# Performance work log

Measured on AMD Instinct MI355X. Metric: run time of the kernel, lower is better.

## Reference

```python
import math
import jax, jax.numpy as jnp
import numpy as np

B = 8          # number of graphs in the batch
NMAX = 256     # max nodes per graph (padding size)
K = 128        # num_kernels
H = 32         # num_heads
NTYPE = 101    # max_node_type + 1


def setup_inputs() -> dict:
    key = jax.random.key(0)
    ks = jax.random.split(key, 10)
    sizes = np.asarray(NMAX - np.arange(B) * 16, dtype=np.int32)  # 256,240,...,144 -> ragged
    N = int(sizes.sum())  # 1600
    coord = jax.random.normal(ks[0], (N, 3), dtype=jnp.float32) * 3.0
    node_type = jax.random.randint(ks[1], (N,), 0, NTYPE, dtype=jnp.int32)
    gaussian_means = jax.random.uniform(ks[2], (1, K), minval=0.0, maxval=3.0, dtype=jnp.float32)
    gaussian_stds = jax.random.uniform(ks[3], (1, K), minval=0.0, maxval=3.0, dtype=jnp.float32)
    # nn.Embedding(max_node_type+1, 2) tables; original init is const(0)/const(1),
    # we perturb so the computation is non-degenerate.
    mul_w = jax.random.normal(ks[4], (NTYPE, 2), dtype=jnp.float32) * 0.1
    bias_w = 1.0 + jax.random.normal(ks[5], (NTYPE, 2), dtype=jnp.float32) * 0.1
    W1 = jax.random.normal(ks[6], (K, K), dtype=jnp.float32) / math.sqrt(K)
    b1 = jnp.zeros((K,), dtype=jnp.float32)
    W2 = jax.random.normal(ks[7], (K, H), dtype=jnp.float32) / math.sqrt(K)
    b2 = jnp.zeros((H,), dtype=jnp.float32)
    return {
        "coord": coord,
        "gaussian_means": gaussian_means,
        "gaussian_stds": gaussian_stds,
        "mul_w": mul_w,
        "bias_w": bias_w,
        "W1": W1,
        "b1": b1,
        "W2": W2,
        "b2": b2,
        "node_type": node_type,
        "batch_num_nodes": jnp.asarray(sizes),
    }


def reference(coord, gaussian_means, gaussian_stds, mul_w, bias_w, W1, b1, W2, b2,
              node_type, batch_num_nodes):
    N = coord.shape[0]
    offsets = jnp.concatenate([jnp.zeros((1,), dtype=batch_num_nodes.dtype),
                               jnp.cumsum(batch_num_nodes)[:-1]])
    ar = jnp.arange(NMAX)
    idx = offsets[:, None] + ar[None, :]                     # [B, n] flat node index per graph slot
    valid = ar[None, :] < batch_num_nodes[:, None]           # [B, n] node mask
    idx_c = jnp.clip(idx, 0, N - 1)
    pc = coord[idx_c]                                        # [B, n, 3] padded coords
    pt = node_type[idx_c]                                    # [B, n]

    # pairwise Euclidean distance (torch.cdist p=2), sqrt-safe at 0
    diff = pc[:, :, None, :] - pc[:, None, :, :]             # [B, n, n, 3]
    sq = jnp.sum(diff * diff, axis=-1)                       # [B, n, n]
    nz = sq > 0
    dist = jnp.where(nz, jnp.sqrt(jnp.where(nz, sq, 1.0)), 0.0)

    # outer-sum of per-node (src, dst) scaling embeddings
    mul_e = mul_w[pt]                                        # [B, n, 2]
    bias_e = bias_w[pt]
    mul = mul_e[:, :, None, 0] + mul_e[:, None, :, 1]        # [B, n, n]
    bias = bias_e[:, :, None, 0] + bias_e[:, None, :, 1]
    scaled = mul * dist + bias                               # [B, n, n]

    means = gaussian_means.reshape(-1)                       # [K]
    stds = jnp.abs(gaussian_stds.reshape(-1)) + 0.01         # [K]
    z = (scaled[..., None] - means) / stds                   # [B, n, n, K]
    gk = jnp.exp(-0.5 * z * z) / (-math.sqrt(2.0 * math.pi) * stds)

    h = jax.nn.gelu(gk @ W1 + b1, approximate=False)         # exact gelu like torch F.gelu
    out = h @ W2 + b2                                        # [B, n, n, H]

    pair = valid[:, :, None] & valid[:, None, :]             # padded positions -> -inf
    return jnp.where(pair[..., None], out, -jnp.inf)
```

## Files before the change

### kernel.cpp

```cpp
#include <hip/hip_runtime.h>
#include <math.h>

#define NMAXC 256
#define KC 128
#define HC 32
#define BC 8
#define TP 128
#define NEG_SENTINEL (-1.0e30f)
#define LOG2E 1.4426950408889634f

typedef __bf16 bf16x8 __attribute__((ext_vector_type(8)));
typedef float  f32x16 __attribute__((ext_vector_type(16)));
union FragU { uint4 u; bf16x8 v; };

#if __has_builtin(__builtin_amdgcn_exp2f)
#define EXP2F(x) __builtin_amdgcn_exp2f(x)
#else
#define EXP2F(x) exp2f(x)
#endif

__device__ __forceinline__ unsigned pack2(float lo, float hi) {
    return __builtin_amdgcn_perm(__float_as_uint(hi), __float_as_uint(lo), 0x07060302u);
}

__device__ __forceinline__ int swap23(int k) {
    return (k & ~12) | ((k & 4) << 1) | ((k & 8) >> 1);
}

__global__ __launch_bounds__(256) void se3d_prep(const float* __restrict__ W1,
                                                 const float* __restrict__ W2,
                                                 const float* __restrict__ gm,
                                                 const float* __restrict__ gs,
                                                 unsigned* __restrict__ wsu) {
    int t = blockIdx.x * 256 + threadIdx.x;
    if (t < 2048) {
        int fb = t >> 6, lane = t & 63;
        int nt = fb >> 3, ks = fb & 7;
        int n  = nt * 32 + (lane & 31);
        int k0 = ks * 16 + 8 * (lane >> 5);
        unsigned u[4];
#pragma unroll
        for (int p = 0; p < 4; ++p)
            u[p] = pack2(W1[(k0 + 2 * p) * KC + n], W1[(k0 + 2 * p + 1) * KC + n]);
        ((uint4*)wsu)[t] = make_uint4(u[0], u[1], u[2], u[3]);
    } else if (t < 2560) {
        int c = t - 2048;
        int ks = c >> 6, lane = c & 63;
        int n  = lane & 31;
        int k0 = ks * 16 + 8 * (lane >> 5);
        unsigned u[4];
#pragma unroll
        for (int p = 0; p < 4; ++p) {
            int ta = swap23(k0 + 2 * p);
            int tb = swap23(k0 + 2 * p + 1);
            u[p] = pack2(W2[ta * HC + n], W2[tb * HC + n]);
        }
        ((uint4*)wsu)[2048 + c] = make_uint4(u[0], u[1], u[2], u[3]);
    } else if (t < 2688) {
        int k = t - 2560;
        float inv = 1.0f / (fabsf(gs[k]) + 0.01f);
        float m  = gm[k];
        float A2 = -0.5f * inv * inv * LOG2E;
        float* wf = (float*)wsu + 10240;
        wf[k]       = A2;
        wf[128 + k] = -2.0f * A2 * m;
        wf[256 + k] = A2 * m * m;
        wf[384 + k] = -0.3989422804014327f * inv;
    }
}

__global__ __launch_bounds__(256, 4) void se3d_main(
    const float* __restrict__ coord, const float* __restrict__ mulw,
    const float* __restrict__ biasw, const float* __restrict__ b1,
    const float* __restrict__ b2, const int* __restrict__ ntype,
    const int* __restrict__ bnn, const void* __restrict__ ws,
    float* __restrict__ out)
{
    __shared__ float scaled[TP];
    __shared__ int   obase[TP];
    __shared__ float cA[KC], cB[KC], cC[KC], cS[KC];

    const int b = blockIdx.y;
    const int n = bnn[b];
    const int q0 = blockIdx.x * TP;
    const int tid = threadIdx.x;

    if (q0 >= n * n) {
        int v = q0 + (tid >> 1) - n * n;
        int wdt = 256 - n;
        int na = n * wdt;
        int i, j;
        if (v < na) { i = v / wdt; j = n + (v - i * wdt); }
        else        { int vp = v - na; i = n + (vp >> 8); j = vp & 255; }
        float4 s4 = make_float4(NEG_SENTINEL, NEG_SENTINEL, NEG_SENTINEL, NEG_SENTINEL);
        float4* o = (float4*)(out + ((size_t)((b * NMAXC + i) * NMAXC + j)) * HC)
                  + (tid & 1) * 4;
#pragma unroll
        for (int t = 0; t < 4; ++t) o[t] = s4;
        return;
    }

    int off = 0;
    for (int t = 0; t < b; ++t) off += bnn[t];

    const float* wf = (const float*)((const char*)ws + 40960);
    if (tid < KC) {
        cA[tid] = wf[tid];
        cB[tid] = wf[128 + tid];
        cC[tid] = wf[256 + tid];
        cS[tid] = wf[384 + tid];
        int q = q0 + tid;
        int i = q / n;
        int j = q - i * n;
        int gi = off + i, gj = off + j;
        float dx = coord[gi * 3 + 0] - coord[gj * 3 + 0];
        float dy = coord[gi * 3 + 1] - coord[gj * 3 + 1];
        float dz = coord[gi * 3 + 2] - coord[gj * 3 + 2];
        float sq = dx * dx + dy * dy + dz * dz;
        float dist = sq > 0.f ? sqrtf(sq) : 0.f;
        int ti = ntype[gi], tj = ntype[gj];
        scaled[tid] = (mulw[ti * 2 + 0] + mulw[tj * 2 + 1]) * dist
                    + (biasw[ti * 2 + 0] + biasw[tj * 2 + 1]);
        obase[tid]  = ((b * NMAXC + i) * NMAXC + j) * HC;
    }
    __syncthreads();

    const int l = tid & 63, w = tid >> 6;
    const int hi = l >> 5, ln31 = l & 31;
    const int m0 = w * 32;
    const float s = scaled[m0 + ln31];

    const bf16x8* wsW1 = (const bf16x8*)ws;
    const bf16x8* wsW2 = (const bf16x8*)((const char*)ws + 32768);
    const float4* A4 = (const float4*)cA;
    const float4* B4 = (const float4*)cB;
    const float4* C4 = (const float4*)cC;
    const float4* S4 = (const float4*)cS;

    f32x16 acc[4];
#pragma unroll
    for (int nt = 0; nt < 4; ++nt) {
#pragma unroll
        for (int g = 0; g < 4; ++g) {
            float4 t4 = *(const float4*)(b1 + nt * 32 + 8 * g + 4 * hi);
            acc[nt][4 * g + 0] = t4.x; acc[nt][4 * g + 1] = t4.y;
            acc[nt][4 * g + 2] = t4.z; acc[nt][4 * g + 3] = t4.w;
        }
    }

#pragma unroll
    for (int ks = 0; ks < 8; ++ks) {
        int b4 = ks * 4 + 2 * hi;
        float4 a0 = A4[b4], a1 = A4[b4 + 1];
        float4 q0v = B4[b4], q1 = B4[b4 + 1];
        float4 c0 = C4[b4], c1 = C4[b4 + 1];
        float4 s0 = S4[b4], s1 = S4[b4 + 1];
        float g[8];
        g[0] = s0.x * EXP2F(fmaf(fmaf(a0.x, s, q0v.x), s, c0.x));
        g[1] = s0.y * EXP2F(fmaf(fmaf(a0.y, s, q0v.y), s, c0.y));
        g[2] = s0.z * EXP2F(fmaf(fmaf(a0.z, s, q0v.z), s, c0.z));
        g[3] = s0.w * EXP2F(fmaf(fmaf(a0.w, s, q0v.w), s, c0.w));
        g[4] = s1.x * EXP2F(fmaf(fmaf(a1.x, s, q1.x), s, c1.x));
        g[5] = s1.y * EXP2F(fmaf(fmaf(a1.y, s, q1.y), s, c1.y));
        g[6] = s1.z * EXP2F(fmaf(fmaf(a1.z, s, q1.z), s, c1.z));
        g[7] = s1.w * EXP2F(fmaf(fmaf(a1.w, s, q1.w), s, c1.w));
        FragU a;
        a.u.x = pack2(g[0], g[1]);
        a.u.y = pack2(g[2], g[3]);
        a.u.z = pack2(g[4], g[5]);
        a.u.w = pack2(g[6], g[7]);
#pragma unroll
        for (int nt = 0; nt < 4; ++nt) {
            bf16x8 bb = wsW1[(nt * 8 + ks) * 64 + l];
            acc[nt] = __builtin_amdgcn_mfma_f32_32x32x16_bf16(bb, a.v, acc[nt], 0, 0, 0);
        }
    }

    f32x16 c2;
#pragma unroll
    for (int g = 0; g < 4; ++g) {
        float4 t4 = *(const float4*)(b2 + 8 * g + 4 * hi);
        c2[4 * g + 0] = t4.x; c2[4 * g + 1] = t4.y;
        c2[4 * g + 2] = t4.z; c2[4 * g + 3] = t4.w;
    }

    const float KSG = -1.702f * LOG2E;
#pragma unroll
    for (int nt = 0; nt < 4; ++nt) {
        float v[16];
#pragma unroll
        for (int r = 0; r < 16; ++r) {
            float x = acc[nt][r];
            float e = EXP2F(x * KSG);
            v[r] = x * __builtin_amdgcn_rcpf(1.0f + e);
        }
        FragU f0, f1;
        f0.u.x = pack2(v[0],  v[1]);  f0.u.y = pack2(v[2],  v[3]);
        f0.u.z = pack2(v[4],  v[5]);  f0.u.w = pack2(v[6],  v[7]);
        f1.u.x = pack2(v[8],  v[9]);  f1.u.y = pack2(v[10], v[11]);
        f1.u.z = pack2(v[12], v[13]); f1.u.w = pack2(v[14], v[15]);
        c2 = __builtin_amdgcn_mfma_f32_32x32x16_bf16(wsW2[(2 * nt + 0) * 64 + l], f0.v, c2, 0, 0, 0);
        c2 = __builtin_amdgcn_mfma_f32_32x32x16_bf16(wsW2[(2 * nt + 1) * 64 + l], f1.v, c2, 0, 0, 0);
    }

    const int ob = obase[m0 + ln31];
    float* op = out + (size_t)ob + 4 * hi;
#pragma unroll
    for (int g = 0; g < 4; ++g) {
        *(float4*)(op + 8 * g) =
            make_float4(c2[4 * g], c2[4 * g + 1], c2[4 * g + 2], c2[4 * g + 3]);
    }
}

extern "C" void kernel_launch(void* const* d_in, const int* in_sizes, int n_in,
                              void* d_out, int out_size, void* d_ws, size_t ws_size,
                              hipStream_t stream) {
    const float* coord = (const float*)d_in[0];
    const float* gm    = (const float*)d_in[1];
    const float* gs    = (const float*)d_in[2];
    const float* mulw  = (const float*)d_in[3];
    const float* biasw = (const float*)d_in[4];
    const float* W1    = (const float*)d_in[5];
    const float* b1    = (const float*)d_in[6];
    const float* W2    = (const float*)d_in[7];
    const float* b2    = (const float*)d_in[8];
    const int* ntype   = (const int*)d_in[9];
    const int* bnn     = (const int*)d_in[10];
    float* out = (float*)d_out;

    hipLaunchKernelGGL(se3d_prep, dim3(11), dim3(256), 0, stream,
                       W1, W2, gm, gs, (unsigned*)d_ws);
    hipLaunchKernelGGL(se3d_main, dim3(NMAXC * NMAXC / TP, BC), dim3(256),
                       0, stream,
                       coord, mulw, biasw, b1, b2, ntype, bnn, d_ws, out);
}
```

Baseline: 125.7 us.

## Fold gaussian scale into exponent, negate W1, and reorder GEMM1/GELU/GEMM2 in halves

Moves the per-kernel normalization factor into the exp2 bias via log2, and negates W1 in the prep kernel to absorb the negative sign. This removes one multiply per gaussian and one shared-memory constant array, and the A and B constants are interleaved so they load as fewer float4 reads. The main loop now builds all eight gaussian fragments first, then computes GEMM1 in two halves of 64 hidden units, each followed by GELU and GEMM2. This keeps fewer accumulators live at once and interleaves MFMA work with exp work, at the cost of holding eight packed fragments in registers.

```diff
diff --git a/kernel.cpp b/kernel.cpp
--- a/kernel.cpp
+++ b/kernel.cpp
@@ -41,7 +41,7 @@
         unsigned u[4];
 #pragma unroll
         for (int p = 0; p < 4; ++p)
-            u[p] = pack2(W1[(k0 + 2 * p) * KC + n], W1[(k0 + 2 * p + 1) * KC + n]);
+            u[p] = pack2(-W1[(k0 + 2 * p) * KC + n], -W1[(k0 + 2 * p + 1) * KC + n]);
         ((uint4*)wsu)[t] = make_uint4(u[0], u[1], u[2], u[3]);
     } else if (t < 2560) {
         int c = t - 2048;
@@ -62,10 +62,9 @@
         float m  = gm[k];
         float A2 = -0.5f * inv * inv * LOG2E;
         float* wf = (float*)wsu + 10240;
-        wf[k]       = A2;
-        wf[128 + k] = -2.0f * A2 * m;
-        wf[256 + k] = A2 * m * m;
-        wf[384 + k] = -0.3989422804014327f * inv;
+        wf[2 * k]     = A2;
+        wf[2 * k + 1] = -2.0f * A2 * m;
+        wf[256 + k]   = A2 * m * m + log2f(0.3989422804014327f * inv);
     }
 }
 
@@ -78,7 +77,8 @@
 {
     __shared__ float scaled[TP];
     __shared__ int   obase[TP];
-    __shared__ float cA[KC], cB[KC], cC[KC], cS[KC];
+    __shared__ float cAB[2 * KC];
+    __shared__ float cC[KC];
 
     const int b = blockIdx.y;
     const int n = bnn[b];
@@ -104,11 +104,9 @@
     for (int t = 0; t < b; ++t) off += bnn[t];
 
     const float* wf = (const float*)((const char*)ws + 40960);
+    if (tid < 2 * KC) cAB[tid] = wf[tid];
     if (tid < KC) {
-        cA[tid] = wf[tid];
-        cB[tid] = wf[128 + tid];
         cC[tid] = wf[256 + tid];
-        cS[tid] = wf[384 + tid];
         int q = q0 + tid;
         int i = q / n;
         int j = q - i * n;
@@ -132,50 +130,30 @@
 
     const bf16x8* wsW1 = (const bf16x8*)ws;
     const bf16x8* wsW2 = (const bf16x8*)((const char*)ws + 32768);
-    const float4* A4 = (const float4*)cA;
-    const float4* B4 = (const float4*)cB;
-    const float4* C4 = (const float4*)cC;
-    const float4* S4 = (const float4*)cS;
-
-    f32x16 acc[4];
-#pragma unroll
-    for (int nt = 0; nt < 4; ++nt) {
-#pragma unroll
-        for (int g = 0; g < 4; ++g) {
-            float4 t4 = *(const float4*)(b1 + nt * 32 + 8 * g + 4 * hi);
-            acc[nt][4 * g + 0] = t4.x; acc[nt][4 * g + 1] = t4.y;
-            acc[nt][4 * g + 2] = t4.z; acc[nt][4 * g + 3] = t4.w;
-        }
-    }
-
+
+    FragU gfr[8];
 #pragma unroll
     for (int ks = 0; ks < 8; ++ks) {
-        int b4 = ks * 4 + 2 * hi;
-        float4 a0 = A4[b4], a1 = A4[b4 + 1];
-        float4 q0v = B4[b4], q1 = B4[b4 + 1];
-        float4 c0 = C4[b4], c1 = C4[b4 + 1];
-        float4 s0 = S4[b4], s1 = S4[b4 + 1];
-        float g[8];
-        g[0] = s0.x * EXP2F(fmaf(fmaf(a0.x, s, q0v.x), s, c0.x));
-        g[1] = s0.y * EXP2F(fmaf(fmaf(a0.y, s, q0v.y), s, c0.y));
-        g[2] = s0.z * EXP2F(fmaf(fmaf(a0.z, s, q0v.z), s, c0.z));
-        g[3] = s0.w * EXP2F(fmaf(fmaf(a0.w, s, q0v.w), s, c0.w));
-        g[4] = s1.x * EXP2F(fmaf(fmaf(a1.x, s, q1.x), s, c1.x));
-        g[5] = s1.y * EXP2F(fmaf(fmaf(a1.y, s, q1.y), s, c1.y));
-        g[6] = s1.z * EXP2F(fmaf(fmaf(a1.z, s, q1.z), s, c1.z));
-        g[7] = s1.w * EXP2F(fmaf(fmaf(a1.w, s, q1.w), s, c1.w));
-        FragU a;
-        a.u.x = pack2(g[0], g[1]);
-        a.u.y = pack2(g[2], g[3]);
-        a.u.z = pack2(g[4], g[5]);
-        a.u.w = pack2(g[6], g[7]);
-#pragma unroll
-        for (int nt = 0; nt < 4; ++nt) {
-            bf16x8 bb = wsW1[(nt * 8 + ks) * 64 + l];
-            acc[nt] = __builtin_amdgcn_mfma_f32_32x32x16_bf16(bb, a.v, acc[nt], 0, 0, 0);
-        }
-    }
-
+        int k0 = ks * 16 + 8 * hi;
+        const float4* ab = (const float4*)(cAB + 2 * k0);
+        const float4* cc = (const float4*)(cC + k0);
+        float4 ab0 = ab[0], ab1 = ab[1], ab2 = ab[2], ab3 = ab[3];
+        float4 c0 = cc[0], c1 = cc[1];
+        float t0 = EXP2F(fmaf(fmaf(ab0.x, s, ab0.y), s, c0.x));
+        float t1 = EXP2F(fmaf(fmaf(ab0.z, s, ab0.w), s, c0.y));
+        float t2 = EXP2F(fmaf(fmaf(ab1.x, s, ab1.y), s, c0.z));
+        float t3 = EXP2F(fmaf(fmaf(ab1.z, s, ab1.w), s, c0.w));
+        float t4 = EXP2F(fmaf(fmaf(ab2.x, s, ab2.y), s, c1.x));
+        float t5 = EXP2F(fmaf(fmaf(ab2.z, s, ab2.w), s, c1.y));
+        float t6 = EXP2F(fmaf(fmaf(ab3.x, s, ab3.y), s, c1.z));
+        float t7 = EXP2F(fmaf(fmaf(ab3.z, s, ab3.w), s, c1.w));
+        gfr[ks].u.x = pack2(t0, t1);
+        gfr[ks].u.y = pack2(t2, t3);
+        gfr[ks].u.z = pack2(t4, t5);
+        gfr[ks].u.w = pack2(t6, t7);
+    }
+
+    const float KSG = -1.702f * LOG2E;
     f32x16 c2;
 #pragma unroll
     for (int g = 0; g < 4; ++g) {
@@ -184,24 +162,48 @@
         c2[4 * g + 2] = t4.z; c2[4 * g + 3] = t4.w;
     }
 
-    const float KSG = -1.702f * LOG2E;
-#pragma unroll
-    for (int nt = 0; nt < 4; ++nt) {
-        float v[16];
-#pragma unroll
-        for (int r = 0; r < 16; ++r) {
-            float x = acc[nt][r];
-            float e = EXP2F(x * KSG);
-            v[r] = x * __builtin_amdgcn_rcpf(1.0f + e);
+#define GELU_PACK(AA, F0, F1) do {                                      \
+    float vv[16];                                                       \
+    _Pragma("unroll")                                                   \
+    for (int r = 0; r < 16; ++r) {                                      \
+        float x = AA[r];                                                \
+        float e = EXP2F(x * KSG);                                       \
+        vv[r] = x * __builtin_amdgcn_rcpf(1.0f + e);                    \
+    }                                                                   \
+    F0.u.x = pack2(vv[0],  vv[1]);  F0.u.y = pack2(vv[2],  vv[3]);      \
+    F0.u.z = pack2(vv[4],  vv[5]);  F0.u.w = pack2(vv[6],  vv[7]);      \
+    F1.u.x = pack2(vv[8],  vv[9]);  F1.u.y = pack2(vv[10], vv[11]);     \
+    F1.u.z = pack2(vv[12], vv[13]); F1.u.w = pack2(vv[14], vv[15]);     \
+} while (0)
+
+#pragma unroll
+    for (int tp = 0; tp < 2; ++tp) {
+        f32x16 a0, a1;
+#pragma unroll
+        for (int g = 0; g < 4; ++g) {
+            float4 t0 = *(const float4*)(b1 + (2 * tp)     * 32 + 8 * g + 4 * hi);
+            float4 t1 = *(const float4*)(b1 + (2 * tp + 1) * 32 + 8 * g + 4 * hi);
+            a0[4 * g + 0] = t0.x; a0[4 * g + 1] = t0.y;
+            a0[4 * g + 2] = t0.z; a0[4 * g + 3] = t0.w;
+            a1[4 * g + 0] = t1.x; a1[4 * g + 1] = t1.y;
+            a1[4 * g + 2] = t1.z; a1[4 * g + 3] = t1.w;
         }
-        FragU f0, f1;
-        f0.u.x = pack2(v[0],  v[1]);  f0.u.y = pack2(v[2],  v[3]);
-        f0.u.z = pack2(v[4],  v[5]);  f0.u.w = pack2(v[6],  v[7]);
-        f1.u.x = pack2(v[8],  v[9]);  f1.u.y = pack2(v[10], v[11]);
-        f1.u.z = pack2(v[12], v[13]); f1.u.w = pack2(v[14], v[15]);
-        c2 = __builtin_amdgcn_mfma_f32_32x32x16_bf16(wsW2[(2 * nt + 0) * 64 + l], f0.v, c2, 0, 0, 0);
-        c2 = __builtin_amdgcn_mfma_f32_32x32x16_bf16(wsW2[(2 * nt + 1) * 64 + l], f1.v, c2, 0, 0, 0);
-    }
+#pragma unroll
+        for (int ks = 0; ks < 8; ++ks) {
+            bf16x8 w0 = wsW1[((2 * tp)     * 8 + ks) * 64 + l];
+            bf16x8 w1 = wsW1[((2 * tp + 1) * 8 + ks) * 64 + l];
+            a0 = __builtin_amdgcn_mfma_f32_32x32x16_bf16(w0, gfr[ks].v, a0, 0, 0, 0);
+            a1 = __builtin_amdgcn_mfma_f32_32x32x16_bf16(w1, gfr[ks].v, a1, 0, 0, 0);
+        }
+        FragU f00, f01, f10, f11;
+        GELU_PACK(a0, f00, f01);
+        GELU_PACK(a1, f10, f11);
+        c2 = __builtin_amdgcn_mfma_f32_32x32x16_bf16(wsW2[(4 * tp + 0) * 64 + l], f00.v, c2, 0, 0, 0);
+        c2 = __builtin_amdgcn_mfma_f32_32x32x16_bf16(wsW2[(4 * tp + 1) * 64 + l], f01.v, c2, 0, 0, 0);
+        c2 = __builtin_amdgcn_mfma_f32_32x32x16_bf16(wsW2[(4 * tp + 2) * 64 + l], f10.v, c2, 0, 0, 0);
+        c2 = __builtin_amdgcn_mfma_f32_32x32x16_bf16(wsW2[(4 * tp + 3) * 64 + l], f11.v, c2, 0, 0, 0);
+    }
+#undef GELU_PACK
 
     const int ob = obase[m0 + ln31];
     float* op = out + (size_t)ob + 4 * hi;
```

Measured after the change: 122.6 us. 1.03x faster.
